# Performance work log

Measured on AMD Instinct MI355X. Metric: run time of the kernel, lower is better.

Reference implementation:

```python
import jax, jax.numpy as jnp
import numpy as np

B, S, D = 1, 1024, 1024
NH, NKV, HD = 16, 4, 64
E, K, HE = 64, 6, 512
EPS = 1e-5


def rmsnorm(x, w, eps=EPS):
    return w * (x * jax.lax.rsqrt(jnp.mean(x * x, axis=-1, keepdims=True) + eps))


def rope(x, cos, sin):
    # x: [b, s, h, hd]; cos/sin: [s, hd//2]; pairs are consecutive elements
    x2 = x.reshape(*x.shape[:-1], -1, 2)
    x0, x1 = x2[..., 0], x2[..., 1]
    c = cos[None, :, None, :]
    s = sin[None, :, None, :]
    o0 = x0 * c - x1 * s
    o1 = x0 * s + x1 * c
    return jnp.stack([o0, o1], axis=-1).reshape(x.shape)


def swiglu(x, w1, w3, w2):
    return (jax.nn.silu(x @ w1) * (x @ w3)) @ w2


def setup_inputs() -> dict:
    key = jax.random.key(0)
    ks = jax.random.split(key, 12)

    def w(k, shape, fan_in):
        return jax.random.normal(k, shape, jnp.float32) / np.sqrt(fan_in).astype(np.float32)

    # RoPE tables (theta = 10000), shape [S, HD//2]
    inv = 1.0 / (10000.0 ** (np.arange(0, HD, 2, dtype=np.float32) / HD))
    ang = np.arange(S, dtype=np.float32)[:, None] * inv[None, :]
    return {
        "x": jax.random.normal(ks[0], (B, S, D), jnp.float32),
        "freqs_cos": jnp.asarray(np.cos(ang), jnp.float32),
        "freqs_sin": jnp.asarray(np.sin(ang), jnp.float32),
        "attn_norm_w": jnp.ones((D,), jnp.float32),
        "ffn_norm_w": jnp.ones((D,), jnp.float32),
        "wq": w(ks[1], (D, NH * HD), D),
        "wk": w(ks[2], (D, NKV * HD), D),
        "wv": w(ks[3], (D, NKV * HD), D),
        "wo": w(ks[4], (NH * HD, D), NH * HD),
        "q_norm_w": jnp.ones((HD,), jnp.float32),
        "k_norm_w": jnp.ones((HD,), jnp.float32),
        "gate_w": w(ks[5], (D, E), D),
        "w1_e": w(ks[6], (E, D, HE), D),
        "w3_e": w(ks[7], (E, D, HE), D),
        "w2_e": w(ks[8], (E, HE, D), HE),
        "sw1": w(ks[9], (D, HE), D),
        "sw3": w(ks[10], (D, HE), D),
        "sw2": w(ks[11], (HE, D), HE),
    }


def reference(x, freqs_cos, freqs_sin, attn_norm_w, ffn_norm_w, wq, wk, wv, wo,
              q_norm_w, k_norm_w, gate_w, w1_e, w3_e, w2_e, sw1, sw3, sw2):
    b, s, d = x.shape
    # ---- attention (GQA + RoPE, causal) ----
    hx = rmsnorm(x, attn_norm_w)
    q = (hx @ wq).reshape(b, s, NH, HD)
    k = (hx @ wk).reshape(b, s, NKV, HD)
    v = (hx @ wv).reshape(b, s, NKV, HD)
    q = rmsnorm(q, q_norm_w)
    k = rmsnorm(k, k_norm_w)
    q = rope(q, freqs_cos, freqs_sin)
    k = rope(k, freqs_cos, freqs_sin)
    n_rep = NH // NKV
    k = jnp.repeat(k, n_rep, axis=2)  # [b,s,NH,HD]
    v = jnp.repeat(v, n_rep, axis=2)
    scores = jnp.einsum("bqhd,bkhd->bhqk", q, k) / jnp.float32(np.sqrt(HD))
    causal = jnp.tril(jnp.ones((s, s), bool))
    scores = jnp.where(causal[None, None], scores, jnp.finfo(scores.dtype).min)
    attn = jax.nn.softmax(scores, axis=-1)
    o = jnp.einsum("bhqk,bkhd->bqhd", attn, v).reshape(b, s, NH * HD) @ wo
    h = x + o

    # ---- MoE SwiGLU (top-k routing, renormalized) ----
    z = rmsnorm(h, ffn_norm_w).reshape(-1, d)  # [T, D]
    T = z.shape[0]
    probs = jax.nn.softmax(z @ gate_w, axis=-1)  # [T, E]
    topw, sel = jax.lax.top_k(probs, K)
    topw = topw / jnp.sum(topw, axis=-1, keepdims=True)
    # dense combine matrix C[t,e] = routing weight (0 if not selected)
    C = jnp.zeros((T, E), z.dtype).at[jnp.arange(T)[:, None], sel].add(topw)
    # expert SwiGLU, combine weights applied before the down-projection
    h1 = jnp.einsum("td,edh->teh", z, w1_e)
    h3 = jnp.einsum("td,edh->teh", z, w3_e)
    g = (jax.nn.silu(h1) * h3) * C[:, :, None]
    moe_out = jnp.einsum("teh,ehd->td", g, w2_e)
    shared = swiglu(z, sw1, sw3, sw2)
    return h + (moe_out + shared).reshape(b, s, d)
```

## Files before the change

### kernel.cpp

```cpp
#include <hip/hip_runtime.h>
#include <hip/hip_bf16.h>
#include <math.h>

#define D_MODEL 1024
#define SEQ     1024
#define NHEADS  16
#define NKVH    4
#define HDIM    64
#define NEXP    64
#define TOPK    6
#define HEXP    512
#define EPS     1e-5f
#define MAXTILES 120

typedef __attribute__((ext_vector_type(8))) short bf16x8;
typedef __attribute__((ext_vector_type(4))) float f32x4;

struct bfrag2 { bf16x8 hi, lo; };
struct f32x8r { float v[8]; };

__device__ __forceinline__ unsigned rne1(float a) {
  union { float f; unsigned u; } x; x.f = a;
  return (x.u + 0x7fffu + ((x.u >> 16) & 1u)) >> 16;
}
__device__ __forceinline__ float frombf(unsigned h) {
  union { float f; unsigned u; } x; x.u = h << 16; return x.f;
}
__device__ __forceinline__ void split_pack(float a, float b, unsigned& hi, unsigned& lo) {
  unsigned ha = rne1(a), hb = rne1(b);
  hi = ha | (hb << 16);
  lo = rne1(a - frombf(ha)) | (rne1(b - frombf(hb)) << 16);
}
__device__ __forceinline__ unsigned pk2bf(float a, float b) {
  return rne1(a) | (rne1(b) << 16);
}

__device__ __forceinline__ f32x4 mfma16(bf16x8 a, bf16x8 b, f32x4 c) {
  return __builtin_amdgcn_mfma_f32_16x16x32_bf16(a, b, c, 0, 0, 0);
}
__device__ __forceinline__ f32x4 mfma_sp(bf16x8 ah, bf16x8 al, const bfrag2& b, f32x4 c) {
  c = mfma16(ah, b.hi, c);
  c = mfma16(ah, b.lo, c);
  c = mfma16(al, b.hi, c);
  return c;
}

__device__ __forceinline__ f32x8r loadraw8(const float* __restrict__ p, int ld) {
  f32x8r r;
#pragma unroll
  for (int i = 0; i < 8; i++) r.v[i] = p[(size_t)ld * i];
  return r;
}
__device__ __forceinline__ bf16x8 cvt_bf(const f32x8r& f) {
  union { bf16x8 v; unsigned u[4]; } r;
  r.u[0] = pk2bf(f.v[0], f.v[1]); r.u[1] = pk2bf(f.v[2], f.v[3]);
  r.u[2] = pk2bf(f.v[4], f.v[5]); r.u[3] = pk2bf(f.v[6], f.v[7]);
  return r.v;
}
__device__ __forceinline__ bfrag2 cvt_bf2(const f32x8r& f) {
  union { bf16x8 v; unsigned u[4]; } H, L;
  split_pack(f.v[0], f.v[1], H.u[0], L.u[0]);
  split_pack(f.v[2], f.v[3], H.u[1], L.u[1]);
  split_pack(f.v[4], f.v[5], H.u[2], L.u[2]);
  split_pack(f.v[6], f.v[7], H.u[3], L.u[3]);
  bfrag2 r; r.hi = H.v; r.lo = L.v; return r;
}

__global__ __launch_bounds__(256) void rmsnorm_k(const float* __restrict__ x,
    const float* __restrict__ w, float* __restrict__ out, ushort* __restrict__ outb) {
  int t = blockIdx.x;
  const float4* xr = (const float4*)(x + (size_t)t * D_MODEL);
  float4 v = xr[threadIdx.x];
  float ss = v.x*v.x + v.y*v.y + v.z*v.z + v.w*v.w;
  for (int off = 32; off; off >>= 1) ss += __shfl_xor(ss, off);
  __shared__ float red[4];
  if ((threadIdx.x & 63) == 0) red[threadIdx.x >> 6] = ss;
  __syncthreads();
  float tot = red[0] + red[1] + red[2] + red[3];
  float inv = rsqrtf(tot * (1.f / D_MODEL) + EPS);
  float4 wv = ((const float4*)w)[threadIdx.x];
  float4 o;
  o.x = v.x * inv * wv.x; o.y = v.y * inv * wv.y;
  o.z = v.z * inv * wv.z; o.w = v.w * inv * wv.w;
  ((float4*)(out + (size_t)t * D_MODEL))[threadIdx.x] = o;
  if (outb) {
    uint2 b;
    b.x = pk2bf(o.x, o.y); b.y = pk2bf(o.z, o.w);
    *(uint2*)(outb + (size_t)t * D_MODEL + threadIdx.x * 4) = b;
  }
}

__global__ __launch_bounds__(256) void mfma_gemm_k(const float* __restrict__ A,
    const float* __restrict__ B, float* __restrict__ C, float* __restrict__ C2,
    const float* __restrict__ resid, int N, int K) {
  __shared__ short Ah[2][16][40];
  __shared__ short Al[2][16][40];
  int bm = blockIdx.y << 4, bn = blockIdx.x << 7;
  int tid = threadIdx.x, wv = tid >> 6, lane = tid & 63;
  int m_ = tid >> 4, k_ = (tid & 15) << 1;
  int arow = lane & 15, akb = (lane >> 4) << 3;
  int c0 = bn + wv * 32 + arow;
  const float* ar = A + (size_t)(bm + m_) * K + k_;
  {
    float2 a2 = *(const float2*)ar;
    unsigned hi, lo; split_pack(a2.x, a2.y, hi, lo);
    *(unsigned*)&Ah[0][m_][k_] = hi;
    *(unsigned*)&Al[0][m_][k_] = lo;
  }
  f32x8r b0r = loadraw8(B + (size_t)akb * N + c0, N);
  f32x8r b1r = loadraw8(B + (size_t)akb * N + c0 + 16, N);
  __syncthreads();
  f32x4 acc0 = {0.f,0.f,0.f,0.f}, acc1 = {0.f,0.f,0.f,0.f};
  int cur = 0;
  for (int k0 = 0; k0 < K; k0 += 32) {
    int kp = (k0 + 32 < K) ? k0 + 32 : 0;
    float2 a2n = *(const float2*)(ar + kp);
    f32x8r b0n = loadraw8(B + (size_t)(kp + akb) * N + c0, N);
    f32x8r b1n = loadraw8(B + (size_t)(kp + akb) * N + c0 + 16, N);
    bfrag2 bf0 = cvt_bf2(b0r), bf1 = cvt_bf2(b1r);
    bf16x8 ah = *(const bf16x8*)&Ah[cur][arow][akb];
    bf16x8 al = *(const bf16x8*)&Al[cur][arow][akb];
    acc0 = mfma_sp(ah, al, bf0, acc0);
    acc1 = mfma_sp(ah, al, bf1, acc1);
    unsigned hi, lo; split_pack(a2n.x, a2n.y, hi, lo);
    *(unsigned*)&Ah[cur ^ 1][m_][k_] = hi;
    *(unsigned*)&Al[cur ^ 1][m_][k_] = lo;
    __syncthreads();
    b0r = b0n; b1r = b1n; cur ^= 1;
  }
  int r0 = (lane >> 4) << 2;
#pragma unroll
  for (int ri = 0; ri < 4; ri++) {
    int row = bm + r0 + ri;
    size_t o0 = (size_t)row * N + c0;
    float v0 = acc0[ri], v1 = acc1[ri];
    if (resid) { v0 += resid[o0]; v1 += resid[o0 + 16]; }
    C[o0] = v0; C[o0 + 16] = v1;
    if (C2) { C2[o0] = v0; C2[o0 + 16] = v1; }
  }
}

__global__ __launch_bounds__(64) void qknorm_rope_k(float* __restrict__ qb,
    float* __restrict__ kb, const float* __restrict__ qw, const float* __restrict__ kw,
    const float* __restrict__ fcos, const float* __restrict__ fsin) {
  int t = blockIdx.x, hid = blockIdx.y, lane = threadIdx.x;
  float* p; const float* w;
  if (hid < NHEADS) { p = qb + (size_t)t * (NHEADS*HDIM) + hid * HDIM; w = qw; }
  else              { p = kb + (size_t)t * (NKVH*HDIM) + (hid - NHEADS) * HDIM; w = kw; }
  float v = p[lane];
  float ss = v * v;
  for (int off = 32; off; off >>= 1) ss += __shfl_xor(ss, off);
  float vn = v * rsqrtf(ss * (1.f / HDIM) + EPS) * w[lane];
  int pi = lane >> 1;
  float c = fcos[t * (HDIM/2) + pi], s = fsin[t * (HDIM/2) + pi];
  float other = __shfl_xor(vn, 1);
  float o = (lane & 1) ? (other * s + vn * c) : (vn * c - other * s);
  p[lane] = o;
}

__global__ __launch_bounds__(256) void attn_mfma(const float* __restrict__ qb,
    const float* __restrict__ kb, const float* __restrict__ vb, float* __restrict__ ob) {
  int h = blockIdx.y;
  int qbase = blockIdx.x << 6;
  int kvh = h >> 2;
  int tid = threadIdx.x, wv = tid >> 6, lane = tid & 63;
  __shared__ short Kt[64][72];
  __shared__ short Vt[64][72];
  __shared__ short Pl[4][16][72];
  int arow = lane & 15;
  int akb = (lane >> 4) << 3;
  int kg = lane >> 4;
  int qrow_base = qbase + wv * 16;
  bf16x8 qf[2];
  {
    const float* qp = qb + (size_t)(qrow_base + arow) * (NHEADS*HDIM) + h * HDIM;
#pragma unroll
    for (int c = 0; c < 2; c++) {
      int d0 = akb + c * 32;
      union { bf16x8 v; unsigned u[4]; } r;
#pragma unroll
      for (int j = 0; j < 4; j++) r.u[j] = pk2bf(qp[d0 + 2*j], qp[d0 + 2*j + 1]);
      qf[c] = r.v;
    }
  }
  f32x4 accO[4];
  float m_[4], l_[4];
#pragma unroll
  for (int n = 0; n < 4; n++) { accO[n] = (f32x4){0.f,0.f,0.f,0.f}; m_[n] = -1e30f; l_[n] = 0.f; }
  int ntiles = (qbase >> 6) + 1;
  for (int ti = 0; ti < ntiles; ti++) {
    int ts = ti << 6;
#pragma unroll
    for (int i = 0; i < 16; i++) {
      int flat = tid + i * 256;
      int kk = flat >> 6, dd = flat & 63;
      size_t src = (size_t)(ts + kk) * (NKVH*HDIM) + kvh * HDIM + dd;
      Kt[kk][dd] = (short)rne1(kb[src]);
      Vt[dd][kk] = (short)rne1(vb[src]);
    }
    __syncthreads();
    f32x4 accS[4];
#pragma unroll
    for (int n = 0; n < 4; n++) accS[n] = (f32x4){0.f,0.f,0.f,0.f};
#pragma unroll
    for (int c = 0; c < 2; c++) {
#pragma unroll
      for (int n = 0; n < 4; n++) {
        bf16x8 bf = *(const bf16x8*)&Kt[n*16 + arow][c*32 + akb];
        accS[n] = mfma16(qf[c], bf, accS[n]);
      }
    }
#pragma unroll
    for (int ri = 0; ri < 4; ri++) {
      int qrow = qrow_base + kg*4 + ri;
      float mx = -1e30f;
#pragma unroll
      for (int n = 0; n < 4; n++) {
        int key = ts + n*16 + arow;
        float s = (key <= qrow) ? accS[n][ri] * 0.125f : -1e30f;
        accS[n][ri] = s;
        mx = fmaxf(mx, s);
      }
      for (int off = 1; off < 16; off <<= 1) mx = fmaxf(mx, __shfl_xor(mx, off));
      float mn = fmaxf(m_[ri], mx);
      float a = __expf(m_[ri] - mn);
      float sum = 0.f;
#pragma unroll
      for (int n = 0; n < 4; n++) {
        float p = __expf(accS[n][ri] - mn);
        accS[n][ri] = p;
        sum += p;
      }
      for (int off = 1; off < 16; off <<= 1) sum += __shfl_xor(sum, off);
      l_[ri] = l_[ri] * a + sum;
      m_[ri] = mn;
#pragma unroll
      for (int n = 0; n < 4; n++) accO[n][ri] *= a;
    }
#pragma unroll
    for (int ri = 0; ri < 4; ri++)
#pragma unroll
      for (int n = 0; n < 4; n++)
        Pl[wv][kg*4 + ri][n*16 + arow] = (short)rne1(accS[n][ri]);
#pragma unroll
    for (int c = 0; c < 2; c++) {
      bf16x8 pf = *(const bf16x8*)&Pl[wv][arow][c*32 + akb];
#pragma unroll
      for (int n = 0; n < 4; n++) {
        bf16x8 vf = *(const bf16x8*)&Vt[n*16 + arow][c*32 + akb];
        accO[n] = mfma16(pf, vf, accO[n]);
      }
    }
    __syncthreads();
  }
#pragma unroll
  for (int ri = 0; ri < 4; ri++) {
    int qrow = qrow_base + kg*4 + ri;
    float inv = 1.f / l_[ri];
#pragma unroll
    for (int n = 0; n < 4; n++)
      ob[(size_t)qrow * (NHEADS*HDIM) + h * HDIM + n*16 + arow] = accO[n][ri] * inv;
  }
}

__global__ __launch_bounds__(64) void gate_topk_k(const float* __restrict__ z,
    const float* __restrict__ gw, int* __restrict__ sel, float* __restrict__ topw,
    int* __restrict__ counts) {
  int t = blockIdx.x, lane = threadIdx.x;
  const float* zr = z + (size_t)t * D_MODEL;
  float acc = 0.f;
  for (int d = 0; d < D_MODEL; d += 4) {
    float4 zv = *(const float4*)(zr + d);
    acc += zv.x * gw[(size_t)(d + 0) * NEXP + lane];
    acc += zv.y * gw[(size_t)(d + 1) * NEXP + lane];
    acc += zv.z * gw[(size_t)(d + 2) * NEXP + lane];
    acc += zv.w * gw[(size_t)(d + 3) * NEXP + lane];
  }
  float m = acc;
  for (int off = 32; off; off >>= 1) m = fmaxf(m, __shfl_xor(m, off));
  float p = __expf(acc - m);
  float s = p;
  for (int off = 32; off; off >>= 1) s += __shfl_xor(s, off);
  p /= s;
  float rem = p, wsum = 0.f;
  float wvv[TOPK]; int wi[TOPK];
  for (int i = 0; i < TOPK; i++) {
    float v = rem; int idx = lane;
    for (int off = 32; off; off >>= 1) {
      float v2 = __shfl_xor(v, off);
      int i2 = __shfl_xor(idx, off);
      if (v2 > v || (v2 == v && i2 < idx)) { v = v2; idx = i2; }
    }
    wvv[i] = v; wi[i] = idx; wsum += v;
    if (lane == idx) rem = -1.f;
  }
  if (lane < TOPK) {
    sel[t * TOPK + lane] = wi[lane];
    topw[t * TOPK + lane] = wvv[lane] / wsum;
  }
  if (lane == 0)
    for (int i = 0; i < TOPK; i++) atomicAdd(&counts[wi[i]], 1);
}

__global__ void scan_k(const int* __restrict__ counts, int* __restrict__ offs,
                       int* __restrict__ cursor, int* __restrict__ tile2e,
                       int* __restrict__ tile2mt, int* __restrict__ ntiles) {
  int lane = threadIdx.x;
  int c = counts[lane];
  int x = c;
  for (int off = 1; off < 64; off <<= 1) {
    int y = __shfl_up(x, off);
    if (lane >= off) x += y;
  }
  offs[lane] = x - c;
  cursor[lane] = x - c;
  int nt = (c + 127) >> 7;
  int y = nt;
  for (int off = 1; off < 64; off <<= 1) {
    int t2 = __shfl_up(y, off);
    if (lane >= off) y += t2;
  }
  int tbase = y - nt;
  for (int i = 0; i < nt; i++) { tile2e[tbase + i] = lane; tile2mt[tbase + i] = i; }
  if (lane == 63) {
    for (int i = 0; i < 8; i++) { tile2e[y + i] = NEXP; tile2mt[y + i] = i; }
    ntiles[0] = y + 8;
  }
}

__global__ void scatter_k(const int* __restrict__ sel, const float* __restrict__ topw,
    int* __restrict__ cursor, int* __restrict__ tok, float* __restrict__ wt) {
  int t = blockIdx.x * 256 + threadIdx.x;
  if (t >= SEQ) return;
  for (int i = 0; i < TOPK; i++) {
    int e = sel[t * TOPK + i];
    int pos = atomicAdd(&cursor[e], 1);
    tok[pos] = t;
    wt[pos] = topw[t * TOPK + i];
  }
}

__global__ __launch_bounds__(256) void moe_up4(const ushort* __restrict__ zb,
    const float* __restrict__ w1, const float* __restrict__ w3, size_t wstride,
    const float* __restrict__ sw1, const float* __restrict__ sw3,
    ushort* __restrict__ g, ushort* __restrict__ sg,
    const int* __restrict__ tok_list, const float* __restrict__ wt_list,
    const int* __restrict__ counts, const int* __restrict__ offs,
    const int* __restrict__ tile2e, const int* __restrict__ tile2mt,
    const int* __restrict__ ntiles) {
  int gt = blockIdx.y;
  if (gt >= ntiles[0]) return;
  int e = tile2e[gt];
  int mt = tile2mt[gt] << 7;
  bool sh = (e == NEXP);
  int cnt = sh ? SEQ : counts[e];
  int off = sh ? 0 : offs[e];
  const float* w1p = sh ? sw1 : w1 + (size_t)e * wstride;
  const float* w3p = sh ? sw3 : w3 + (size_t)e * wstride;
  ushort* gout = sh ? sg : g;
  __shared__ ushort Ah[2][128][40];
  __shared__ int toks[128];
  int tid = threadIdx.x, wv = tid >> 6, lane = tid & 63;
  int arow = lane & 15, akb = (lane >> 4) << 3, kg = lane >> 4;
  int c0 = (blockIdx.x << 6) + wv * 16 + arow;
  if (tid < 128) {
    int r = mt + tid; if (r >= cnt) r = cnt - 1;
    toks[tid] = sh ? r : tok_list[off + r];
  }
  __syncthreads();
  int row0 = tid >> 2, q8 = (tid & 3) * 8;
  int row1 = row0 + 64;
  {
    uint4 a0 = *(const uint4*)(zb + (size_t)toks[row0] * D_MODEL + q8);
    uint4 a1v = *(const uint4*)(zb + (size_t)toks[row1] * D_MODEL + q8);
    *(uint4*)&Ah[0][row0][q8] = a0;
    *(uint4*)&Ah[0][row1][q8] = a1v;
  }
  f32x8r b1r = loadraw8(w1p + (size_t)akb * HEXP + c0, HEXP);
  f32x8r b3r = loadraw8(w3p + (size_t)akb * HEXP + c0, HEXP);
  __syncthreads();
  f32x4 a1[8], a3[8];
#pragma unroll
  for (int f = 0; f < 8; f++) { a1[f] = (f32x4){0.f,0.f,0.f,0.f}; a3[f] = (f32x4){0.f,0.f,0.f,0.f}; }
  int cur = 0;
  for (int k0 = 0; k0 < D_MODEL; k0 += 32) {
    int kp = (k0 + 32 < D_MODEL) ? k0 + 32 : 0;
    uint4 an0 = *(const uint4*)(zb + (size_t)toks[row0] * D_MODEL + kp + q8);
    uint4 an1 = *(const uint4*)(zb + (size_t)toks[row1] * D_MODEL + kp + q8);
    f32x8r b1n = loadraw8(w1p + (size_t)(kp + akb) * HEXP + c0, HEXP);
    f32x8r b3n = loadraw8(w3p + (size_t)(kp + akb) * HEXP + c0, HEXP);
    bf16x8 b1 = cvt_bf(b1r), b3 = cvt_bf(b3r);
#pragma unroll
    for (int f = 0; f < 8; f++) {
      bf16x8 ah = *(const bf16x8*)&Ah[cur][f*16 + arow][akb];
      a1[f] = mfma16(ah, b1, a1[f]);
      a3[f] = mfma16(ah, b3, a3[f]);
    }
    *(uint4*)&Ah[cur ^ 1][row0][q8] = an0;
    *(uint4*)&Ah[cur ^ 1][row1][q8] = an1;
    __syncthreads();
    b1r = b1n; b3r = b3n; cur ^= 1;
  }
#pragma unroll
  for (int f = 0; f < 8; f++)
#pragma unroll
    for (int ri = 0; ri < 4; ri++) {
      int r = mt + f*16 + kg*4 + ri;
      if (r < cnt) {
        float wt = sh ? 1.0f : wt_list[off + r];
        float h1 = a1[f][ri], h3 = a3[f][ri];
        float gv = h1 / (1.f + __expf(-h1)) * h3 * wt;
        gout[(size_t)(off + r) * HEXP + c0] = (ushort)rne1(gv);
      }
    }
}

__global__ __launch_bounds__(256) void moe_down4(const ushort* __restrict__ g,
    const ushort* __restrict__ sg, const float* __restrict__ w2, size_t wstride,
    const float* __restrict__ sw2, float* __restrict__ out,
    const int* __restrict__ tok_list, const int* __restrict__ counts,
    const int* __restrict__ offs, const int* __restrict__ tile2e,
    const int* __restrict__ tile2mt, const int* __restrict__ ntiles) {
  int gt = blockIdx.y;
  if (gt >= ntiles[0]) return;
  int e = tile2e[gt];
  int mt = tile2mt[gt] << 7;
  bool sh = (e == NEXP);
  int cnt = sh ? SEQ : counts[e];
  int off = sh ? 0 : offs[e];
  const float* w2p = sh ? sw2 : w2 + (size_t)e * wstride;
  const ushort* gin = sh ? sg : g;
  __shared__ ushort Ah[2][128][40];
  __shared__ int ridx[128];
  int tid = threadIdx.x, wv = tid >> 6, lane = tid & 63;
  int arow = lane & 15, akb = (lane >> 4) << 3, kg = lane >> 4;
  int c0 = (blockIdx.x << 7) + wv * 32 + arow;
  if (tid < 128) {
    int r = mt + tid; if (r >= cnt) r = cnt - 1;
    ridx[tid] = off + r;
  }
  __syncthreads();
  int row0 = tid >> 2, q8 = (tid & 3) * 8;
  int row1 = row0 + 64;
  {
    uint4 a0 = *(const uint4*)(gin + (size_t)ridx[row0] * HEXP + q8);
    uint4 a1v = *(const uint4*)(gin + (size_t)ridx[row1] * HEXP + q8);
    *(uint4*)&Ah[0][row0][q8] = a0;
    *(uint4*)&Ah[0][row1][q8] = a1v;
  }
  f32x8r b0r = loadraw8(w2p + (size_t)akb * D_MODEL + c0, D_MODEL);
  f32x8r b1r = loadraw8(w2p + (size_t)akb * D_MODEL + c0 + 16, D_MODEL);
  __syncthreads();
  f32x4 ac0[8], ac1[8];
#pragma unroll
  for (int f = 0; f < 8; f++) { ac0[f] = (f32x4){0.f,0.f,0.f,0.f}; ac1[f] = (f32x4){0.f,0.f,0.f,0.f}; }
  int cur = 0;
  for (int k0 = 0; k0 < HEXP; k0 += 32) {
    int kp = (k0 + 32 < HEXP) ? k0 + 32 : 0;
    uint4 an0 = *(const uint4*)(gin + (size_t)ridx[row0] * HEXP + kp + q8);
    uint4 an1 = *(const uint4*)(gin + (size_t)ridx[row1] * HEXP + kp + q8);
    f32x8r b0n = loadraw8(w2p + (size_t)(kp + akb) * D_MODEL + c0, D_MODEL);
    f32x8r b1n = loadraw8(w2p + (size_t)(kp + akb) * D_MODEL + c0 + 16, D_MODEL);
    bf16x8 b0 = cvt_bf(b0r), b1 = cvt_bf(b1r);
#pragma unroll
    for (int f = 0; f < 8; f++) {
      bf16x8 ah = *(const bf16x8*)&Ah[cur][f*16 + arow][akb];
      ac0[f] = mfma16(ah, b0, ac0[f]);
      ac1[f] = mfma16(ah, b1, ac1[f]);
    }
    *(uint4*)&Ah[cur ^ 1][row0][q8] = an0;
    *(uint4*)&Ah[cur ^ 1][row1][q8] = an1;
    __syncthreads();
    b0r = b0n; b1r = b1n; cur ^= 1;
  }
#pragma unroll
  for (int f = 0; f < 8; f++)
#pragma unroll
    for (int ri = 0; ri < 4; ri++) {
      int r = mt + f*16 + kg*4 + ri;
      if (r < cnt) {
        int tok = sh ? r : tok_list[off + r];
        float* op = out + (size_t)tok * D_MODEL + c0;
        atomicAdd(op, ac0[f][ri]);
        atomicAdd(op + 16, ac1[f][ri]);
      }
    }
}

extern "C" void kernel_launch(void* const* d_in, const int* in_sizes, int n_in,
                              void* d_out, int out_size, void* d_ws, size_t ws_size,
                              hipStream_t stream) {
  const float* x     = (const float*)d_in[0];
  const float* fcos  = (const float*)d_in[1];
  const float* fsin  = (const float*)d_in[2];
  const float* anw   = (const float*)d_in[3];
  const float* fnw   = (const float*)d_in[4];
  const float* wq    = (const float*)d_in[5];
  const float* wk    = (const float*)d_in[6];
  const float* wvv   = (const float*)d_in[7];
  const float* wo    = (const float*)d_in[8];
  const float* qnw   = (const float*)d_in[9];
  const float* knw   = (const float*)d_in[10];
  const float* gatew = (const float*)d_in[11];
  const float* w1e   = (const float*)d_in[12];
  const float* w3e   = (const float*)d_in[13];
  const float* w2e   = (const float*)d_in[14];
  const float* sw1   = (const float*)d_in[15];
  const float* sw3   = (const float*)d_in[16];
  const float* sw2   = (const float*)d_in[17];
  float* out = (float*)d_out;

  char* ws = (char*)d_ws;
  const size_t MB = 1ull << 20;
  float*  hx    = (float*)(ws);
  float*  h     = (float*)(ws + 4*MB);
  float*  z     = (float*)(ws + 8*MB);
  float*  qbuf  = (float*)(ws + 12*MB);
  float*  kbuf  = (float*)(ws + 16*MB);
  float*  vbuf  = (float*)(ws + 17*MB);
  ushort* zb    = (ushort*)(ws + 12*MB);
  ushort* gb    = (ushort*)(ws + 14*MB);
  ushort* s_gb  = (ushort*)(ws + 20*MB + 512*1024);
  char*   misc  = ws + 22*MB;
  int*   sel      = (int*)(misc);
  float* topw     = (float*)(misc + 24576);
  int*   counts   = (int*)(misc + 49152);
  int*   offs     = (int*)(misc + 49408);
  int*   cursor   = (int*)(misc + 49664);
  int*   ntiles   = (int*)(misc + 50432);
  int*   tile2e   = (int*)(misc + 50688);
  int*   tile2mt  = (int*)(misc + 51200);
  int*   tok_list = (int*)(misc + 51712);
  float* wt_list  = (float*)(misc + 76288);

  rmsnorm_k<<<SEQ, 256, 0, stream>>>(x, anw, hx, nullptr);
  mfma_gemm_k<<<dim3(8, 64), 256, 0, stream>>>(hx, wq, qbuf, nullptr, nullptr, 1024, 1024);
  mfma_gemm_k<<<dim3(2, 64), 256, 0, stream>>>(hx, wk, kbuf, nullptr, nullptr, 256, 1024);
  mfma_gemm_k<<<dim3(2, 64), 256, 0, stream>>>(hx, wvv, vbuf, nullptr, nullptr, 256, 1024);
  qknorm_rope_k<<<dim3(SEQ, NHEADS + NKVH), 64, 0, stream>>>(qbuf, kbuf, qnw, knw, fcos, fsin);
  attn_mfma<<<dim3(SEQ / 64, NHEADS), 256, 0, stream>>>(qbuf, kbuf, vbuf, hx);
  mfma_gemm_k<<<dim3(8, 64), 256, 0, stream>>>(hx, wo, h, out, x, 1024, 1024);
  rmsnorm_k<<<SEQ, 256, 0, stream>>>(h, fnw, z, zb);
  hipMemsetAsync(counts, 0, 256, stream);
  gate_topk_k<<<SEQ, 64, 0, stream>>>(z, gatew, sel, topw, counts);
  scan_k<<<1, 64, 0, stream>>>(counts, offs, cursor, tile2e, tile2mt, ntiles);
  scatter_k<<<SEQ / 256, 256, 0, stream>>>(sel, topw, cursor, tok_list, wt_list);
  moe_up4<<<dim3(HEXP / 64, MAXTILES), 256, 0, stream>>>(zb, w1e, w3e,
      (size_t)D_MODEL * HEXP, sw1, sw3, gb, s_gb, tok_list, wt_list,
      counts, offs, tile2e, tile2mt, ntiles);
  moe_down4<<<dim3(D_MODEL / 128, MAXTILES), 256, 0, stream>>>(gb, s_gb, w2e,
      (size_t)HEXP * D_MODEL, sw2, out, tok_list, counts, offs,
      tile2e, tile2mt, ntiles);
  (void)in_sizes; (void)n_in; (void)out_size; (void)ws_size;
}
```

Measured before the change: 425.2 us.

## Deepen global-load prefetch to two K-steps in GEMM and MoE kernels

The dense GEMM and both MoE grouped GEMMs now keep register prefetches two K-steps ahead, using even and odd register sets and a loop manually unrolled by two, instead of one step ahead. This gives more latency hiding for the fp32 weight loads and the gathered activation loads. moe_down also drops the shared ridx table and its extra barrier, computing row pointers directly, and the gather row pointers are hoisted out of the loop. The cost is higher register pressure from doubled in-flight buffers, which may lower occupancy.

```diff
diff --git a/kernel.cpp b/kernel.cpp
--- a/kernel.cpp
+++ b/kernel.cpp
@@ -102,31 +102,52 @@
   int c0 = bn + wv * 32 + arow;
   const float* ar = A + (size_t)(bm + m_) * K + k_;
   {
-    float2 a2 = *(const float2*)ar;
-    unsigned hi, lo; split_pack(a2.x, a2.y, hi, lo);
+    float2 a0 = *(const float2*)ar;
+    unsigned hi, lo; split_pack(a0.x, a0.y, hi, lo);
     *(unsigned*)&Ah[0][m_][k_] = hi;
     *(unsigned*)&Al[0][m_][k_] = lo;
   }
-  f32x8r b0r = loadraw8(B + (size_t)akb * N + c0, N);
-  f32x8r b1r = loadraw8(B + (size_t)akb * N + c0 + 16, N);
+  float2 aO = *(const float2*)(ar + 32);
+  float2 aE;
+  f32x8r bE0 = loadraw8(B + (size_t)akb * N + c0, N);
+  f32x8r bE1 = loadraw8(B + (size_t)akb * N + c0 + 16, N);
+  f32x8r bO0 = loadraw8(B + (size_t)(32 + akb) * N + c0, N);
+  f32x8r bO1 = loadraw8(B + (size_t)(32 + akb) * N + c0 + 16, N);
   __syncthreads();
   f32x4 acc0 = {0.f,0.f,0.f,0.f}, acc1 = {0.f,0.f,0.f,0.f};
-  int cur = 0;
-  for (int k0 = 0; k0 < K; k0 += 32) {
-    int kp = (k0 + 32 < K) ? k0 + 32 : 0;
-    float2 a2n = *(const float2*)(ar + kp);
-    f32x8r b0n = loadraw8(B + (size_t)(kp + akb) * N + c0, N);
-    f32x8r b1n = loadraw8(B + (size_t)(kp + akb) * N + c0 + 16, N);
-    bfrag2 bf0 = cvt_bf2(b0r), bf1 = cvt_bf2(b1r);
-    bf16x8 ah = *(const bf16x8*)&Ah[cur][arow][akb];
-    bf16x8 al = *(const bf16x8*)&Al[cur][arow][akb];
-    acc0 = mfma_sp(ah, al, bf0, acc0);
-    acc1 = mfma_sp(ah, al, bf1, acc1);
-    unsigned hi, lo; split_pack(a2n.x, a2n.y, hi, lo);
-    *(unsigned*)&Ah[cur ^ 1][m_][k_] = hi;
-    *(unsigned*)&Al[cur ^ 1][m_][k_] = lo;
-    __syncthreads();
-    b0r = b0n; b1r = b1n; cur ^= 1;
+  for (int k0 = 0; k0 < K; k0 += 64) {
+    {
+      int kp = (k0 + 64 < K) ? k0 + 64 : 0;
+      f32x8r n0 = loadraw8(B + (size_t)(kp + akb) * N + c0, N);
+      f32x8r n1 = loadraw8(B + (size_t)(kp + akb) * N + c0 + 16, N);
+      float2 an = *(const float2*)(ar + kp);
+      bfrag2 f0 = cvt_bf2(bE0), f1 = cvt_bf2(bE1);
+      bf16x8 ah = *(const bf16x8*)&Ah[0][arow][akb];
+      bf16x8 al = *(const bf16x8*)&Al[0][arow][akb];
+      acc0 = mfma_sp(ah, al, f0, acc0);
+      acc1 = mfma_sp(ah, al, f1, acc1);
+      unsigned hi, lo; split_pack(aO.x, aO.y, hi, lo);
+      *(unsigned*)&Ah[1][m_][k_] = hi;
+      *(unsigned*)&Al[1][m_][k_] = lo;
+      __syncthreads();
+      bE0 = n0; bE1 = n1; aE = an;
+    }
+    {
+      int kp = (k0 + 96 < K) ? k0 + 96 : 0;
+      f32x8r n0 = loadraw8(B + (size_t)(kp + akb) * N + c0, N);
+      f32x8r n1 = loadraw8(B + (size_t)(kp + akb) * N + c0 + 16, N);
+      float2 an = *(const float2*)(ar + kp);
+      bfrag2 f0 = cvt_bf2(bO0), f1 = cvt_bf2(bO1);
+      bf16x8 ah = *(const bf16x8*)&Ah[1][arow][akb];
+      bf16x8 al = *(const bf16x8*)&Al[1][arow][akb];
+      acc0 = mfma_sp(ah, al, f0, acc0);
+      acc1 = mfma_sp(ah, al, f1, acc1);
+      unsigned hi, lo; split_pack(aE.x, aE.y, hi, lo);
+      *(unsigned*)&Ah[0][m_][k_] = hi;
+      *(unsigned*)&Al[0][m_][k_] = lo;
+      __syncthreads();
+      bO0 = n0; bO1 = n1; aO = an;
+    }
   }
   int r0 = (lane >> 4) << 2;
 #pragma unroll
@@ -340,7 +361,7 @@
   }
 }
 
-__global__ __launch_bounds__(256) void moe_up4(const ushort* __restrict__ zb,
+__global__ __launch_bounds__(256) void moe_up5(const ushort* __restrict__ zb,
     const float* __restrict__ w1, const float* __restrict__ w3, size_t wstride,
     const float* __restrict__ sw1, const float* __restrict__ sw3,
     ushort* __restrict__ g, ushort* __restrict__ sg,
@@ -370,36 +391,62 @@
   __syncthreads();
   int row0 = tid >> 2, q8 = (tid & 3) * 8;
   int row1 = row0 + 64;
+  const ushort* zr0 = zb + (size_t)toks[row0] * D_MODEL + q8;
+  const ushort* zr1 = zb + (size_t)toks[row1] * D_MODEL + q8;
   {
-    uint4 a0 = *(const uint4*)(zb + (size_t)toks[row0] * D_MODEL + q8);
-    uint4 a1v = *(const uint4*)(zb + (size_t)toks[row1] * D_MODEL + q8);
-    *(uint4*)&Ah[0][row0][q8] = a0;
-    *(uint4*)&Ah[0][row1][q8] = a1v;
-  }
-  f32x8r b1r = loadraw8(w1p + (size_t)akb * HEXP + c0, HEXP);
-  f32x8r b3r = loadraw8(w3p + (size_t)akb * HEXP + c0, HEXP);
+    uint4 t0 = *(const uint4*)zr0;
+    uint4 t1 = *(const uint4*)zr1;
+    *(uint4*)&Ah[0][row0][q8] = t0;
+    *(uint4*)&Ah[0][row1][q8] = t1;
+  }
+  uint4 aO0 = *(const uint4*)(zr0 + 32);
+  uint4 aO1 = *(const uint4*)(zr1 + 32);
+  uint4 aE0, aE1;
+  f32x8r bE1 = loadraw8(w1p + (size_t)akb * HEXP + c0, HEXP);
+  f32x8r bE3 = loadraw8(w3p + (size_t)akb * HEXP + c0, HEXP);
+  f32x8r bO1 = loadraw8(w1p + (size_t)(32 + akb) * HEXP + c0, HEXP);
+  f32x8r bO3 = loadraw8(w3p + (size_t)(32 + akb) * HEXP + c0, HEXP);
   __syncthreads();
   f32x4 a1[8], a3[8];
 #pragma unroll
   for (int f = 0; f < 8; f++) { a1[f] = (f32x4){0.f,0.f,0.f,0.f}; a3[f] = (f32x4){0.f,0.f,0.f,0.f}; }
-  int cur = 0;
-  for (int k0 = 0; k0 < D_MODEL; k0 += 32) {
-    int kp = (k0 + 32 < D_MODEL) ? k0 + 32 : 0;
-    uint4 an0 = *(const uint4*)(zb + (size_t)toks[row0] * D_MODEL + kp + q8);
-    uint4 an1 = *(const uint4*)(zb + (size_t)toks[row1] * D_MODEL + kp + q8);
-    f32x8r b1n = loadraw8(w1p + (size_t)(kp + akb) * HEXP + c0, HEXP);
-    f32x8r b3n = loadraw8(w3p + (size_t)(kp + akb) * HEXP + c0, HEXP);
-    bf16x8 b1 = cvt_bf(b1r), b3 = cvt_bf(b3r);
-#pragma unroll
-    for (int f = 0; f < 8; f++) {
-      bf16x8 ah = *(const bf16x8*)&Ah[cur][f*16 + arow][akb];
-      a1[f] = mfma16(ah, b1, a1[f]);
-      a3[f] = mfma16(ah, b3, a3[f]);
-    }
-    *(uint4*)&Ah[cur ^ 1][row0][q8] = an0;
-    *(uint4*)&Ah[cur ^ 1][row1][q8] = an1;
-    __syncthreads();
-    b1r = b1n; b3r = b3n; cur ^= 1;
+  for (int k0 = 0; k0 < D_MODEL; k0 += 64) {
+    {
+      int kp = (k0 + 64 < D_MODEL) ? k0 + 64 : 0;
+      f32x8r n1 = loadraw8(w1p + (size_t)(kp + akb) * HEXP + c0, HEXP);
+      f32x8r n3 = loadraw8(w3p + (size_t)(kp + akb) * HEXP + c0, HEXP);
+      uint4 an0 = *(const uint4*)(zr0 + kp);
+      uint4 an1 = *(const uint4*)(zr1 + kp);
+      bf16x8 b1 = cvt_bf(bE1), b3 = cvt_bf(bE3);
+#pragma unroll
+      for (int f = 0; f < 8; f++) {
+        bf16x8 ah = *(const bf16x8*)&Ah[0][f*16 + arow][akb];
+        a1[f] = mfma16(ah, b1, a1[f]);
+        a3[f] = mfma16(ah, b3, a3[f]);
+      }
+      *(uint4*)&Ah[1][row0][q8] = aO0;
+      *(uint4*)&Ah[1][row1][q8] = aO1;
+      __syncthreads();
+      bE1 = n1; bE3 = n3; aE0 = an0; aE1 = an1;
+    }
+    {
+      int kp = (k0 + 96 < D_MODEL) ? k0 + 96 : 0;
+      f32x8r n1 = loadraw8(w1p + (size_t)(kp + akb) * HEXP + c0, HEXP);
+      f32x8r n3 = loadraw8(w3p + (size_t)(kp + akb) * HEXP + c0, HEXP);
+      uint4 an0 = *(const uint4*)(zr0 + kp);
+      uint4 an1 = *(const uint4*)(zr1 + kp);
+      bf16x8 b1 = cvt_bf(bO1), b3 = cvt_bf(bO3);
+#pragma unroll
+      for (int f = 0; f < 8; f++) {
+        bf16x8 ah = *(const bf16x8*)&Ah[1][f*16 + arow][akb];
+        a1[f] = mfma16(ah, b1, a1[f]);
+        a3[f] = mfma16(ah, b3, a3[f]);
+      }
+      *(uint4*)&Ah[0][row0][q8] = aE0;
+      *(uint4*)&Ah[0][row1][q8] = aE1;
+      __syncthreads();
+      bO1 = n1; bO3 = n3; aO0 = an0; aO1 = an1;
+    }
   }
 #pragma unroll
   for (int f = 0; f < 8; f++)
@@ -415,7 +462,7 @@
     }
 }
 
-__global__ __launch_bounds__(256) void moe_down4(const ushort* __restrict__ g,
+__global__ __launch_bounds__(256) void moe_down5(const ushort* __restrict__ g,
     const ushort* __restrict__ sg, const float* __restrict__ w2, size_t wstride,
     const float* __restrict__ sw2, float* __restrict__ out,
     const int* __restrict__ tok_list, const int* __restrict__ counts,
@@ -431,47 +478,69 @@
   const float* w2p = sh ? sw2 : w2 + (size_t)e * wstride;
   const ushort* gin = sh ? sg : g;
   __shared__ ushort Ah[2][128][40];
-  __shared__ int ridx[128];
   int tid = threadIdx.x, wv = tid >> 6, lane = tid & 63;
   int arow = lane & 15, akb = (lane >> 4) << 3, kg = lane >> 4;
   int c0 = (blockIdx.x << 7) + wv * 32 + arow;
-  if (tid < 128) {
-    int r = mt + tid; if (r >= cnt) r = cnt - 1;
-    ridx[tid] = off + r;
-  }
-  __syncthreads();
   int row0 = tid >> 2, q8 = (tid & 3) * 8;
   int row1 = row0 + 64;
+  int rr0 = mt + row0; if (rr0 >= cnt) rr0 = cnt - 1;
+  int rr1 = mt + row1; if (rr1 >= cnt) rr1 = cnt - 1;
+  const ushort* gr0 = gin + (size_t)(off + rr0) * HEXP + q8;
+  const ushort* gr1 = gin + (size_t)(off + rr1) * HEXP + q8;
   {
-    uint4 a0 = *(const uint4*)(gin + (size_t)ridx[row0] * HEXP + q8);
-    uint4 a1v = *(const uint4*)(gin + (size_t)ridx[row1] * HEXP + q8);
-    *(uint4*)&Ah[0][row0][q8] = a0;
-    *(uint4*)&Ah[0][row1][q8] = a1v;
-  }
-  f32x8r b0r = loadraw8(w2p + (size_t)akb * D_MODEL + c0, D_MODEL);
-  f32x8r b1r = loadraw8(w2p + (size_t)akb * D_MODEL + c0 + 16, D_MODEL);
+    uint4 t0 = *(const uint4*)gr0;
+    uint4 t1 = *(const uint4*)gr1;
+    *(uint4*)&Ah[0][row0][q8] = t0;
+    *(uint4*)&Ah[0][row1][q8] = t1;
+  }
+  uint4 aO0 = *(const uint4*)(gr0 + 32);
+  uint4 aO1 = *(const uint4*)(gr1 + 32);
+  uint4 aE0, aE1;
+  f32x8r bEa = loadraw8(w2p + (size_t)akb * D_MODEL + c0, D_MODEL);
+  f32x8r bEb = loadraw8(w2p + (size_t)akb * D_MODEL + c0 + 16, D_MODEL);
+  f32x8r bOa = loadraw8(w2p + (size_t)(32 + akb) * D_MODEL + c0, D_MODEL);
+  f32x8r bOb = loadraw8(w2p + (size_t)(32 + akb) * D_MODEL + c0 + 16, D_MODEL);
   __syncthreads();
   f32x4 ac0[8], ac1[8];
 #pragma unroll
   for (int f = 0; f < 8; f++) { ac0[f] = (f32x4){0.f,0.f,0.f,0.f}; ac1[f] = (f32x4){0.f,0.f,0.f,0.f}; }
-  int cur = 0;
-  for (int k0 = 0; k0 < HEXP; k0 += 32) {
-    int kp = (k0 + 32 < HEXP) ? k0 + 32 : 0;
-    uint4 an0 = *(const uint4*)(gin + (size_t)ridx[row0] * HEXP + kp + q8);
-    uint4 an1 = *(const uint4*)(gin + (size_t)ridx[row1] * HEXP + kp + q8);
-    f32x8r b0n = loadraw8(w2p + (size_t)(kp + akb) * D_MODEL + c0, D_MODEL);
-    f32x8r b1n = loadraw8(w2p + (size_t)(kp + akb) * D_MODEL + c0 + 16, D_MODEL);
-    bf16x8 b0 = cvt_bf(b0r), b1 = cvt_bf(b1r);
-#pragma unroll
-    for (int f = 0; f < 8; f++) {
-      bf16x8 ah = *(const bf16x8*)&Ah[cur][f*16 + arow][akb];
-      ac0[f] = mfma16(ah, b0, ac0[f]);
-      ac1[f] = mfma16(ah, b1, ac1[f]);
-    }
-    *(uint4*)&Ah[cur ^ 1][row0][q8] = an0;
-    *(uint4*)&Ah[cur ^ 1][row1][q8] = an1;
-    __syncthreads();
-    b0r = b0n; b1r = b1n; cur ^= 1;
+  for (int k0 = 0; k0 < HEXP; k0 += 64) {
+    {
+      int kp = (k0 + 64 < HEXP) ? k0 + 64 : 0;
+      f32x8r na = loadraw8(w2p + (size_t)(kp + akb) * D_MODEL + c0, D_MODEL);
+      f32x8r nb = loadraw8(w2p + (size_t)(kp + akb) * D_MODEL + c0 + 16, D_MODEL);
+      uint4 an0 = *(const uint4*)(gr0 + kp);
+      uint4 an1 = *(const uint4*)(gr1 + kp);
+      bf16x8 b0 = cvt_bf(bEa), b1 = cvt_bf(bEb);
+#pragma unroll
+      for (int f = 0; f < 8; f++) {
+        bf16x8 ah = *(const bf16x8*)&Ah[0][f*16 + arow][akb];
+        ac0[f] = mfma16(ah, b0, ac0[f]);
+        ac1[f] = mfma16(ah, b1, ac1[f]);
+      }
+      *(uint4*)&Ah[1][row0][q8] = aO0;
+      *(uint4*)&Ah[1][row1][q8] = aO1;
+      __syncthreads();
+      bEa = na; bEb = nb; aE0 = an0; aE1 = an1;
+    }
+    {
+      int kp = (k0 + 96 < HEXP) ? k0 + 96 : 0;
+      f32x8r na = loadraw8(w2p + (size_t)(kp + akb) * D_MODEL + c0, D_MODEL);
+      f32x8r nb = loadraw8(w2p + (size_t)(kp + akb) * D_MODEL + c0 + 16, D_MODEL);
+      uint4 an0 = *(const uint4*)(gr0 + kp);
+      uint4 an1 = *(const uint4*)(gr1 + kp);
+      bf16x8 b0 = cvt_bf(bOa), b1 = cvt_bf(bOb);
+#pragma unroll
+      for (int f = 0; f < 8; f++) {
+        bf16x8 ah = *(const bf16x8*)&Ah[1][f*16 + arow][akb];
+        ac0[f] = mfma16(ah, b0, ac0[f]);
+        ac1[f] = mfma16(ah, b1, ac1[f]);
+      }
+      *(uint4*)&Ah[0][row0][q8] = aE0;
+      *(uint4*)&Ah[0][row1][q8] = aE1;
+      __syncthreads();
+      bOa = na; bOb = nb; aO0 = an0; aO1 = an1;
+    }
   }
 #pragma unroll
   for (int f = 0; f < 8; f++)
@@ -545,10 +614,10 @@
   gate_topk_k<<<SEQ, 64, 0, stream>>>(z, gatew, sel, topw, counts);
   scan_k<<<1, 64, 0, stream>>>(counts, offs, cursor, tile2e, tile2mt, ntiles);
   scatter_k<<<SEQ / 256, 256, 0, stream>>>(sel, topw, cursor, tok_list, wt_list);
-  moe_up4<<<dim3(HEXP / 64, MAXTILES), 256, 0, stream>>>(zb, w1e, w3e,
+  moe_up5<<<dim3(HEXP / 64, MAXTILES), 256, 0, stream>>>(zb, w1e, w3e,
       (size_t)D_MODEL * HEXP, sw1, sw3, gb, s_gb, tok_list, wt_list,
       counts, offs, tile2e, tile2mt, ntiles);
-  moe_down4<<<dim3(D_MODEL / 128, MAXTILES), 256, 0, stream>>>(gb, s_gb, w2e,
+  moe_down5<<<dim3(D_MODEL / 128, MAXTILES), 256, 0, stream>>>(gb, s_gb, w2e,
       (size_t)HEXP * D_MODEL, sw2, out, tok_list, counts, offs,
       tile2e, tile2mt, ntiles);
   (void)in_sizes; (void)n_in; (void)out_size; (void)ws_size;
```

Measured after the change: 413.3 us. 1.03x faster.
